# Kernel optimization log

Measured on AMD Instinct MI355X. Metric: run time of the kernel, lower is better.

The kernel has to match this reference:

```python
import jax, jax.numpy as jnp
import numpy as np

B, T, S, V, D, H = 32, 50, 40, 32000, 512, 1024


def setup_inputs() -> dict:
    key = jax.random.key(0)
    ks = jax.random.split(key, 14)
    s_ih = 1.0 / np.sqrt(H)
    return {
        "zh_gruths": jax.random.randint(ks[0], (B, T), 0, V),
        "encoder_hs": jax.random.normal(ks[1], (B, S, H), jnp.float32),
        "encoder_h_n": jax.random.normal(ks[2], (1, B, H), jnp.float32) * 0.1,
        "encoder_c_n": jax.random.normal(ks[3], (1, B, H), jnp.float32) * 0.1,
        "entext_len": jax.random.randint(ks[4], (B,), 1, S + 1),
        "teacher_forcing_ratio": 1,
        "emb": jax.random.normal(ks[5], (V, D), jnp.float32) * 0.02,
        "W_ih": jax.random.normal(ks[6], (4 * H, D), jnp.float32) * s_ih,
        "W_hh": jax.random.normal(ks[7], (4 * H, H), jnp.float32) * s_ih,
        "b_ih": jax.random.normal(ks[8], (4 * H,), jnp.float32) * s_ih,
        "b_hh": jax.random.normal(ks[9], (4 * H,), jnp.float32) * s_ih,
        "W_ht": jax.random.normal(ks[10], (H, 2 * H), jnp.float32) * (1.0 / np.sqrt(2 * H)),
        "b_ht": jnp.zeros((H,), jnp.float32),
        "W_voc": jax.random.normal(ks[11], (V, H), jnp.float32) * s_ih,
        "b_voc": jnp.zeros((V,), jnp.float32),
    }


def reference(zh_gruths, encoder_hs, encoder_h_n, encoder_c_n, entext_len,
              teacher_forcing_ratio, emb, W_ih, W_hh, b_ih, b_hh,
              W_ht, b_ht, W_voc, b_voc):
    # teacher_forcing_ratio == 1 -> always teacher forcing (deterministic branch)
    xs = jnp.swapaxes(emb[zh_gruths], 0, 1)  # [T, B, D]
    hx0, cx0 = encoder_h_n[0], encoder_c_n[0]  # [B, H]

    def step(carry, xt):
        hx, cx = carry
        gates = xt @ W_ih.T + b_ih + hx @ W_hh.T + b_hh  # [B, 4H]
        i, f, g, o = jnp.split(gates, 4, axis=-1)  # torch gate order i,f,g,o
        i, f, o = jax.nn.sigmoid(i), jax.nn.sigmoid(f), jax.nn.sigmoid(o)
        cx = f * cx + i * jnp.tanh(g)
        hx = o * jnp.tanh(cx)
        # dot attention over encoder states
        scores = jnp.einsum('bsh,bh->bs', encoder_hs, hx)
        attn = jax.nn.softmax(scores, axis=-1)
        ctx = jnp.einsum('bs,bsh->bh', attn, encoder_hs)
        hx_atten = jnp.tanh(jnp.concatenate([ctx, hx], axis=-1) @ W_ht.T + b_ht)
        logits_t = hx_atten @ W_voc.T + b_voc  # [B, V]
        return (hx, cx), logits_t

    _, logits = jax.lax.scan(step, (hx0, cx0), xs)  # [T, B, V]
    logits = jnp.swapaxes(logits, 0, 1)  # [B, T, V]
    predicts = jnp.argmax(logits, axis=-1)  # [B, T]
    return logits, predicts
```

## Files before the change

kernel.cpp:

```cpp
#include <hip/hip_runtime.h>
#include <math.h>

typedef short bf16x8 __attribute__((ext_vector_type(8)));
typedef float f32x4 __attribute__((ext_vector_type(4)));
typedef float f32x2 __attribute__((ext_vector_type(2)));
typedef unsigned int uint;
typedef uint u32x4 __attribute__((ext_vector_type(4)));
typedef unsigned long long ull;
typedef unsigned short ushort;

#define Bz 32
#define Tz 50
#define Sz 40
#define Vz 32000
#define Dz 512
#define Hz 1024
#define Mz 1600
#define Mp 1664
#define CAP 1024

__device__ __forceinline__ ushort f2bf(float f) {
    uint u = __builtin_bit_cast(uint, f);
    return (ushort)((u + 0x7FFFu + ((u >> 16) & 1u)) >> 16);
}
__device__ __forceinline__ float bf2f(ushort h) {
    uint u = ((uint)h) << 16;
    return __builtin_bit_cast(float, u);
}
__device__ __forceinline__ void splitf(float f, ushort& hi, ushort& lo) {
    uint u = __builtin_bit_cast(uint, f);
    hi = (ushort)(u >> 16);
    float rem = f - __builtin_bit_cast(float, u & 0xFFFF0000u);
    lo = (ushort)(__builtin_bit_cast(uint, rem) >> 16);
}
__device__ __forceinline__ void splitrn(float f, ushort& hi, ushort& lo) {
    hi = f2bf(f);
    lo = f2bf(f - bf2f(hi));
}
__device__ __forceinline__ float sigf(float x) { return 1.f / (1.f + expf(-x)); }

__device__ __forceinline__ uint ld_sc1(const uint* p) {
    uint v;
    asm volatile("global_load_dword %0, %1, off sc0 sc1\n\ts_waitcnt vmcnt(0)"
                 : "=&v"(v) : "v"(p) : "memory");
    return v;
}
__device__ __forceinline__ void st_sc1(uint* p, uint v) {
    asm volatile("global_store_dword %0, %1, off sc0 sc1" :: "v"(p), "v"(v) : "memory");
}

__global__ __launch_bounds__(256) void k_pre(ushort* hxA_hi, ushort* hxA_lo, float* cx,
                                             ushort* AH_hi, ushort* AH_lo, uint* flags,
                                             const float* h0, const float* c0) {
    int gid = blockIdx.x * 256 + threadIdx.x;
    if (gid < 32768) {
        float v = h0[gid];
        ushort hi, lo;
        splitf(v, hi, lo);
        hxA_hi[gid] = hi;
        hxA_lo[gid] = lo;
    } else if (gid < 65536) {
        cx[gid - 32768] = c0[gid - 32768];
    } else if (gid < 196608) {
        int g = gid - 65536;
        AH_hi[(long)Mz * 2048 + g] = 0;
        AH_lo[(long)Mz * 2048 + g] = 0;
    } else if (gid < 196608 + 2048) {
        st_sc1(&flags[gid - 196608], 0u);
    }
}

__global__ __launch_bounds__(256) void k_wsplit(const float* __restrict__ src,
                                                ushort* __restrict__ hi, ushort* __restrict__ lo,
                                                int n4) {
    int stride = gridDim.x * 256;
    for (int i = blockIdx.x * 256 + threadIdx.x; i < n4; i += stride) {
        float4 f = *(const float4*)(src + (long)i * 4);
        float vv[4] = {f.x, f.y, f.z, f.w};
        ushort h[4], l[4];
#pragma unroll
        for (int e = 0; e < 4; ++e) splitf(vv[e], h[e], l[e]);
        uint2 hp, lp;
        hp.x = (uint)h[0] | ((uint)h[1] << 16);
        hp.y = (uint)h[2] | ((uint)h[3] << 16);
        lp.x = (uint)l[0] | ((uint)l[1] << 16);
        lp.y = (uint)l[2] | ((uint)l[3] << 16);
        *(uint2*)(hi + (long)i * 4) = hp;
        *(uint2*)(lo + (long)i * 4) = lp;
    }
}

__global__ __launch_bounds__(256) void k_wbf16(const float* __restrict__ src,
                                               ushort* __restrict__ dst, int n4) {
    int stride = gridDim.x * 256;
    for (int i = blockIdx.x * 256 + threadIdx.x; i < n4; i += stride) {
        float4 f = *(const float4*)(src + (long)i * 4);
        uint2 hp;
        hp.x = (uint)f2bf(f.x) | ((uint)f2bf(f.y) << 16);
        hp.y = (uint)f2bf(f.z) | ((uint)f2bf(f.w) << 16);
        *(uint2*)(dst + (long)i * 4) = hp;
    }
}

__global__ __launch_bounds__(256, 1) void k_xgemm(const float* __restrict__ emb,
                                                  const int* __restrict__ tok,
                                                  const float* __restrict__ Wih,
                                                  const float* __restrict__ bih,
                                                  const float* __restrict__ bhh,
                                                  float* __restrict__ gx) {
    __shared__ ushort sAh[128][40];
    __shared__ ushort sAl[128][40];
    __shared__ ushort sBh[128][40];
    __shared__ ushort sBl[128][40];
    int bid = blockIdx.x;
    int mt = bid >> 5, nt = bid & 31;
    int tid = threadIdx.x;
    int row = tid >> 1, half = tid & 1;
    int wv = tid >> 6, lane = tid & 63;
    int wr = wv >> 1, wc = wv & 1;
    int m0 = wr * 64, n0 = wc * 64;
    int r16 = lane & 15, kg = lane >> 4, k0 = kg * 8;

    f32x4 acc[4][4];
#pragma unroll
    for (int i = 0; i < 4; i++)
#pragma unroll
        for (int j = 0; j < 4; j++) acc[i][j] = (f32x4){0.f, 0.f, 0.f, 0.f};

    int r = mt * 128 + row;
    int tk = (r < Mz) ? tok[r] : 0;
    const float* arow = emb + (long)tk * Dz;
    const float* brow = Wih + (long)(nt * 128 + row) * Dz;

    for (int kb = 0; kb < Dz; kb += 32) {
        {
            ushort hh[16], ll[16];
#pragma unroll
            for (int q = 0; q < 16; q += 4) {
                float4 w4 = (r < Mz) ? *(const float4*)(arow + kb + half * 16 + q)
                                     : (float4){0.f, 0.f, 0.f, 0.f};
                float vv[4] = {w4.x, w4.y, w4.z, w4.w};
#pragma unroll
                for (int e = 0; e < 4; ++e) splitf(vv[e], hh[q + e], ll[q + e]);
            }
            *(uint4*)&sAh[row][half * 16]     = *(uint4*)&hh[0];
            *(uint4*)&sAh[row][half * 16 + 8] = *(uint4*)&hh[8];
            *(uint4*)&sAl[row][half * 16]     = *(uint4*)&ll[0];
            *(uint4*)&sAl[row][half * 16 + 8] = *(uint4*)&ll[8];
        }
        {
            ushort hh[16], ll[16];
#pragma unroll
            for (int q = 0; q < 16; q += 4) {
                float4 w4 = *(const float4*)(brow + kb + half * 16 + q);
                float vv[4] = {w4.x, w4.y, w4.z, w4.w};
#pragma unroll
                for (int e = 0; e < 4; ++e) splitf(vv[e], hh[q + e], ll[q + e]);
            }
            *(uint4*)&sBh[row][half * 16]     = *(uint4*)&hh[0];
            *(uint4*)&sBh[row][half * 16 + 8] = *(uint4*)&hh[8];
            *(uint4*)&sBl[row][half * 16]     = *(uint4*)&ll[0];
            *(uint4*)&sBl[row][half * 16 + 8] = *(uint4*)&ll[8];
        }
        __syncthreads();
        bf16x8 af[4], alf[4], bhf[4], blf[4];
#pragma unroll
        for (int i = 0; i < 4; ++i) {
            af[i]  = *(const bf16x8*)&sAh[m0 + i * 16 + r16][k0];
            alf[i] = *(const bf16x8*)&sAl[m0 + i * 16 + r16][k0];
            bhf[i] = *(const bf16x8*)&sBh[n0 + i * 16 + r16][k0];
            blf[i] = *(const bf16x8*)&sBl[n0 + i * 16 + r16][k0];
        }
#pragma unroll
        for (int i = 0; i < 4; ++i)
#pragma unroll
            for (int jn = 0; jn < 4; ++jn) {
                acc[i][jn] = __builtin_amdgcn_mfma_f32_16x16x32_bf16(af[i],  bhf[jn], acc[i][jn], 0, 0, 0);
                acc[i][jn] = __builtin_amdgcn_mfma_f32_16x16x32_bf16(af[i],  blf[jn], acc[i][jn], 0, 0, 0);
                acc[i][jn] = __builtin_amdgcn_mfma_f32_16x16x32_bf16(alf[i], bhf[jn], acc[i][jn], 0, 0, 0);
            }
        __syncthreads();
    }
#pragma unroll
    for (int i = 0; i < 4; ++i) {
        int gr0 = mt * 128 + m0 + i * 16 + kg * 4;
#pragma unroll
        for (int reg = 0; reg < 4; ++reg) {
            int gr = gr0 + reg;
            if (gr >= Mz) continue;
#pragma unroll
            for (int jn = 0; jn < 4; ++jn) {
                int gc = nt * 128 + n0 + jn * 16 + r16;
                gx[(long)gr * 4096 + gc] = acc[i][jn][reg] + bih[gc] + bhh[gc];
            }
        }
    }
}

__global__ __launch_bounds__(512, 1) void k_recfused7(
    const float* __restrict__ gx,
    const ushort* __restrict__ Whi, const ushort* __restrict__ Wlo,
    ushort* __restrict__ hxA_hi, ushort* __restrict__ hxA_lo,
    float* __restrict__ hxh, float* __restrict__ cx,
    const float* __restrict__ enc,
    ushort* __restrict__ AH_hi, ushort* __restrict__ AH_lo,
    uint* flags,
    const float* __restrict__ Wvoc, ushort* __restrict__ Wvh,
    int do_wsplit) {
    __shared__ u32x4 stg4[8192];
    __shared__ float hxs[Hz];
    __shared__ float sc[64];
    __shared__ float aw[64];
    int wid = blockIdx.x, tid = threadIdx.x;

    if (wid >= 96) {
        if (do_wsplit) {
            int n4 = Vz * Hz / 4;
            int stride = 160 * 512;
            for (int i = (wid - 96) * 512 + tid; i < n4; i += stride) {
                float4 f = *(const float4*)(Wvoc + (long)i * 4);
                uint2 hp;
                hp.x = (uint)f2bf(f.x) | ((uint)f2bf(f.y) << 16);
                hp.y = (uint)f2bf(f.z) | ((uint)f2bf(f.w) << 16);
                *(uint2*)(Wvh + (long)i * 4) = hp;
            }
        }
        return;
    }

    int lane = tid & 63, kh = tid >> 6;

    for (int t = 0; t <= Tz; ++t) {
        if (wid < 64) {
            if (t < Tz) {
                int w = wid;
                int p = t & 1, q = p ^ 1;
                {
                    bool done = false;
                    while (!done) {
                        uint f = 0xFFFFFFFFu;
                        if (lane < 8) f = ld_sc1(&flags[(kh * 8 + lane) * 16]);
                        done = (bool)__all(f >= (uint)t);
                        if (!done) __builtin_amdgcn_s_sleep(1);
                    }
                }
                int kslot = kh * 16 + (lane & 15);
                int rowb = (lane >> 4) * 8;
                const ushort* planes[2] = { hxA_hi + p * 32768, hxA_lo + p * 32768 };
#pragma unroll
                for (int plane = 0; plane < 2; ++plane) {
                    const ushort* b0 = planes[plane] + (long)rowb * 1024 + kslot * 8;
                    u32x4 d0, d1, d2, d3, d4, d5, d6, d7;
                    asm volatile(
                        "global_load_dwordx4 %0, %8, off sc0 sc1\n\t"
                        "global_load_dwordx4 %1, %9, off sc0 sc1\n\t"
                        "global_load_dwordx4 %2, %10, off sc0 sc1\n\t"
                        "global_load_dwordx4 %3, %11, off sc0 sc1\n\t"
                        "global_load_dwordx4 %4, %12, off sc0 sc1\n\t"
                        "global_load_dwordx4 %5, %13, off sc0 sc1\n\t"
                        "global_load_dwordx4 %6, %14, off sc0 sc1\n\t"
                        "global_load_dwordx4 %7, %15, off sc0 sc1\n\t"
                        "s_waitcnt vmcnt(0)"
                        : "=&v"(d0), "=&v"(d1), "=&v"(d2), "=&v"(d3),
                          "=&v"(d4), "=&v"(d5), "=&v"(d6), "=&v"(d7)
                        : "v"(b0), "v"(b0 + 1024), "v"(b0 + 2048), "v"(b0 + 3072),
                          "v"(b0 + 4096), "v"(b0 + 5120), "v"(b0 + 6144), "v"(b0 + 7168)
                        : "memory");
                    int li = plane * 4096 + kslot * 32;
                    stg4[li + ((rowb + 0 + kslot) & 31)] = d0;
                    stg4[li + ((rowb + 1 + kslot) & 31)] = d1;
                    stg4[li + ((rowb + 2 + kslot) & 31)] = d2;
                    stg4[li + ((rowb + 3 + kslot) & 31)] = d3;
                    stg4[li + ((rowb + 4 + kslot) & 31)] = d4;
                    stg4[li + ((rowb + 5 + kslot) & 31)] = d5;
                    stg4[li + ((rowb + 6 + kslot) & 31)] = d6;
                    stg4[li + ((rowb + 7 + kslot) & 31)] = d7;
                }
                int r16 = lane & 15, kg = lane >> 4;
                int jbase = w * 16 + r16;
                const ushort* whbase = Whi + (long)jbase * 1024;
                const ushort* wlbase = Wlo + (long)jbase * 1024;
                f32x4 acc[2][4];
#pragma unroll
                for (int i = 0; i < 2; ++i)
#pragma unroll
                    for (int v = 0; v < 4; ++v) acc[i][v] = (f32x4){0.f, 0.f, 0.f, 0.f};
#pragma unroll
                for (int it = 0; it < 4; ++it) {
                    int ksl = kh * 16 + it * 4 + kg;
                    int k0 = ksl * 8;
                    bf16x8 a_h0 = *(const bf16x8*)&stg4[       ksl * 32 + ((r16 + ksl) & 31)];
                    bf16x8 a_l0 = *(const bf16x8*)&stg4[4096 + ksl * 32 + ((r16 + ksl) & 31)];
                    bf16x8 a_h1 = *(const bf16x8*)&stg4[       ksl * 32 + ((16 + r16 + ksl) & 31)];
                    bf16x8 a_l1 = *(const bf16x8*)&stg4[4096 + ksl * 32 + ((16 + r16 + ksl) & 31)];
                    bf16x8 bh[4], bl[4];
#pragma unroll
                    for (int v = 0; v < 4; ++v) {
                        bh[v] = *(const bf16x8*)(whbase + ((long)v << 20) + k0);
                        bl[v] = *(const bf16x8*)(wlbase + ((long)v << 20) + k0);
                    }
#pragma unroll
                    for (int v = 0; v < 4; ++v) {
                        acc[0][v] = __builtin_amdgcn_mfma_f32_16x16x32_bf16(a_h0, bh[v], acc[0][v], 0, 0, 0);
                        acc[0][v] = __builtin_amdgcn_mfma_f32_16x16x32_bf16(a_l0, bh[v], acc[0][v], 0, 0, 0);
                        acc[0][v] = __builtin_amdgcn_mfma_f32_16x16x32_bf16(a_h0, bl[v], acc[0][v], 0, 0, 0);
                        acc[1][v] = __builtin_amdgcn_mfma_f32_16x16x32_bf16(a_h1, bh[v], acc[1][v], 0, 0, 0);
                        acc[1][v] = __builtin_amdgcn_mfma_f32_16x16x32_bf16(a_l1, bh[v], acc[1][v], 0, 0, 0);
                        acc[1][v] = __builtin_amdgcn_mfma_f32_16x16x32_bf16(a_h1, bl[v], acc[1][v], 0, 0, 0);
                    }
                }
                __syncthreads();
                float* sgp = (float*)stg4;
#pragma unroll
                for (int i = 0; i < 2; ++i)
#pragma unroll
                    for (int v = 0; v < 4; ++v)
#pragma unroll
                        for (int reg = 0; reg < 4; ++reg)
                            sgp[(((kh * 4 + v) * 32) + i * 16 + kg * 4 + reg) * 16 + r16] = acc[i][v][reg];
                __syncthreads();
                int b = tid >> 4, h16 = tid & 15;
                int hg = w * 16 + h16;
                const float* gxr = gx + ((long)b * Tz + t) * 4096 + hg;
                float g0 = 0.f, g1 = 0.f, g2 = 0.f, g3 = 0.f;
#pragma unroll
                for (int khh = 0; khh < 8; ++khh) {
                    g0 += sgp[((khh * 4 + 0) * 32 + b) * 16 + h16];
                    g1 += sgp[((khh * 4 + 1) * 32 + b) * 16 + h16];
                    g2 += sgp[((khh * 4 + 2) * 32 + b) * 16 + h16];
                    g3 += sgp[((khh * 4 + 3) * 32 + b) * 16 + h16];
                }
                g0 += gxr[0]; g1 += gxr[1024]; g2 += gxr[2048]; g3 += gxr[3072];
                long ci = (long)b * Hz + hg;
                float c = sigf(g1) * cx[ci] + sigf(g0) * tanhf(g2);
                float hv = sigf(g3) * tanhf(c);
                cx[ci] = c;
                float* hp = hxh + ((long)t * Bz + b) * Hz + hg;
                asm volatile("global_store_dword %0, %1, off sc0 sc1" :: "v"(hp), "v"(hv));
                ushort hi, lo;
                splitf(hv, hi, lo);
                ushort* hip = hxA_hi + q * 32768 + ci;
                ushort* lop = hxA_lo + q * 32768 + ci;
                asm volatile("global_store_short %0, %1, off sc0 sc1" :: "v"(hip), "v"((uint)hi));
                asm volatile("global_store_short %0, %1, off sc0 sc1" :: "v"(lop), "v"((uint)lo));
                asm volatile("s_waitcnt vmcnt(0)" ::: "memory");
                __syncthreads();
                if (tid == 0) st_sc1(&flags[wid * 16], (uint)(t + 1));
            }
        } else {
            if (t > 0) {
                int b = wid - 64, tt = t - 1;
                if (tid < 64) {
                    bool done = false;
                    while (!done) {
                        uint f = ld_sc1(&flags[tid * 16]);
                        done = (bool)__all(f >= (uint)t);
                        if (!done) __builtin_amdgcn_s_sleep(2);
                    }
                }
                __syncthreads();
                const float* hsrc = hxh + ((long)tt * Bz + b) * Hz + tid * 2;
                f32x2 h2;
                asm volatile("global_load_dwordx2 %0, %1, off sc0 sc1\n\ts_waitcnt vmcnt(0)"
                             : "=&v"(h2) : "v"(hsrc) : "memory");
                hxs[tid * 2] = h2[0];
                hxs[tid * 2 + 1] = h2[1];
                __syncthreads();
                int wv = tid >> 6;
                float hreg[16];
#pragma unroll
                for (int u = 0; u < 16; ++u) hreg[u] = hxs[lane * 16 + u];
                const float* eb = enc + (long)b * Sz * Hz;
                for (int s = wv; s < Sz; s += 8) {
                    const float* er = eb + (long)s * Hz + lane * 16;
                    float sum = 0.f;
#pragma unroll
                    for (int qq = 0; qq < 4; ++qq) {
                        float4 e4 = *(const float4*)(er + qq * 4);
                        sum += e4.x * hreg[qq*4] + e4.y * hreg[qq*4+1] + e4.z * hreg[qq*4+2] + e4.w * hreg[qq*4+3];
                    }
#pragma unroll
                    for (int off = 32; off >= 1; off >>= 1) sum += __shfl_xor(sum, off);
                    if (lane == 0) sc[s] = sum;
                }
                __syncthreads();
                if (tid < 64) {
                    float vv = (tid < Sz) ? sc[tid] : -3.402823e38f;
                    float mx = vv;
#pragma unroll
                    for (int off = 32; off >= 1; off >>= 1) mx = fmaxf(mx, __shfl_xor(mx, off));
                    float e = (tid < Sz) ? expf(vv - mx) : 0.f;
                    float ssum = e;
#pragma unroll
                    for (int off = 32; off >= 1; off >>= 1) ssum += __shfl_xor(ssum, off);
                    if (tid < Sz) aw[tid] = e / ssum;
                }
                __syncthreads();
                float c0 = 0.f, c1 = 0.f;
#pragma unroll 4
                for (int s = 0; s < Sz; ++s) {
                    float2 e2 = *(const float2*)(eb + (long)s * Hz + tid * 2);
                    float a = aw[s];
                    c0 += a * e2.x; c1 += a * e2.y;
                }
                long rr = (long)b * Tz + tt;
                ushort* dh = AH_hi + rr * 2048;
                ushort* dl = AH_lo + rr * 2048;
                ushort hi, lo;
                splitf(c0, hi, lo); dh[tid * 2]     = hi; dl[tid * 2]     = lo;
                splitf(c1, hi, lo); dh[tid * 2 + 1] = hi; dl[tid * 2 + 1] = lo;
                splitf(hxs[tid * 2],     hi, lo); dh[1024 + tid * 2]     = hi; dl[1024 + tid * 2]     = lo;
                splitf(hxs[tid * 2 + 1], hi, lo); dh[1024 + tid * 2 + 1] = hi; dl[1024 + tid * 2 + 1] = lo;
            }
        }
    }
}

__global__ __launch_bounds__(256, 1) void k_ht(const ushort* __restrict__ Ah,
                                               const ushort* __restrict__ Al,
                                               const ushort* __restrict__ Bh,
                                               const ushort* __restrict__ Bl,
                                               const float* __restrict__ bht,
                                               ushort* __restrict__ Hh, ushort* __restrict__ Hl) {
    __shared__ ushort sAh[128][40];
    __shared__ ushort sAl[128][40];
    __shared__ ushort sBh[128][40];
    __shared__ ushort sBl[128][40];
    int bid = blockIdx.x;
    int mt = bid >> 3, nt = bid & 7;
    int tid = threadIdx.x;
    int row = tid >> 1, half = tid & 1;
    int wv = tid >> 6, lane = tid & 63;
    int wr = wv >> 1, wc = wv & 1;
    int m0 = wr * 64, n0 = wc * 64;
    int r16 = lane & 15, kg = lane >> 4, k0 = kg * 8;

    f32x4 acc[4][4];
#pragma unroll
    for (int i = 0; i < 4; i++)
#pragma unroll
        for (int j = 0; j < 4; j++) acc[i][j] = (f32x4){0.f, 0.f, 0.f, 0.f};

    long arow = (long)(mt * 128 + row) * 2048;
    long brow = (long)(nt * 128 + row) * 2048;

    for (int kb = 0; kb < 2048; kb += 32) {
        const ushort* pa = Ah + arow + kb + half * 16;
        *(uint4*)&sAh[row][half * 16]     = *(const uint4*)pa;
        *(uint4*)&sAh[row][half * 16 + 8] = *(const uint4*)(pa + 8);
        const ushort* pl = Al + arow + kb + half * 16;
        *(uint4*)&sAl[row][half * 16]     = *(const uint4*)pl;
        *(uint4*)&sAl[row][half * 16 + 8] = *(const uint4*)(pl + 8);
        const ushort* pb = Bh + brow + kb + half * 16;
        *(uint4*)&sBh[row][half * 16]     = *(const uint4*)pb;
        *(uint4*)&sBh[row][half * 16 + 8] = *(const uint4*)(pb + 8);
        const ushort* pc = Bl + brow + kb + half * 16;
        *(uint4*)&sBl[row][half * 16]     = *(const uint4*)pc;
        *(uint4*)&sBl[row][half * 16 + 8] = *(const uint4*)(pc + 8);
        __syncthreads();
        bf16x8 af[4], alf[4], bhf[4], blf[4];
#pragma unroll
        for (int i = 0; i < 4; ++i) {
            af[i]  = *(const bf16x8*)&sAh[m0 + i * 16 + r16][k0];
            alf[i] = *(const bf16x8*)&sAl[m0 + i * 16 + r16][k0];
            bhf[i] = *(const bf16x8*)&sBh[n0 + i * 16 + r16][k0];
            blf[i] = *(const bf16x8*)&sBl[n0 + i * 16 + r16][k0];
        }
#pragma unroll
        for (int i = 0; i < 4; ++i)
#pragma unroll
            for (int jn = 0; jn < 4; ++jn) {
                acc[i][jn] = __builtin_amdgcn_mfma_f32_16x16x32_bf16(af[i],  bhf[jn], acc[i][jn], 0, 0, 0);
                acc[i][jn] = __builtin_amdgcn_mfma_f32_16x16x32_bf16(af[i],  blf[jn], acc[i][jn], 0, 0, 0);
                acc[i][jn] = __builtin_amdgcn_mfma_f32_16x16x32_bf16(alf[i], bhf[jn], acc[i][jn], 0, 0, 0);
            }
        __syncthreads();
    }
#pragma unroll
    for (int i = 0; i < 4; ++i) {
        int gr0 = mt * 128 + m0 + i * 16 + kg * 4;
#pragma unroll
        for (int reg = 0; reg < 4; ++reg) {
            int gr = gr0 + reg;
            bool valid = gr < Mz;
#pragma unroll
            for (int jn = 0; jn < 4; ++jn) {
                int gc = nt * 128 + n0 + jn * 16 + r16;
                float vv = tanhf(acc[i][jn][reg] + bht[gc]);
                ushort hi = 0, lo = 0;
                if (valid) splitrn(vv, hi, lo);
                Hh[(long)gr * Hz + gc] = hi;
                Hl[(long)gr * Hz + gc] = lo;
            }
        }
    }
}

__global__ __launch_bounds__(256, 2) void k_voc4(
    const ushort* __restrict__ Ah, const ushort* __restrict__ Wh,
    const float* __restrict__ bvoc,
    float* __restrict__ out, ull* __restrict__ keys) {
    __shared__ ushort sAh[128][40];
    __shared__ ushort sBh[128][40];
    int bid = blockIdx.x;
    int nt = bid % 250, mg = bid / 250;
    int mt_beg = (mg == 0) ? 0 : 7;
    int mt_end = (mg == 0) ? 7 : 13;
    int tid = threadIdx.x;
    int row = tid >> 1, half = tid & 1;
    int wv = tid >> 6, lane = tid & 63;
    int wr = wv >> 1, wc = wv & 1;
    int m0 = wr * 64, n0 = wc * 64;
    int r16 = lane & 15, kg = lane >> 4, k0 = kg * 8;

    long wrow = (long)(nt * 128 + row) * Hz;
    int vcol_base = nt * 128 + n0;

    for (int mt = mt_beg; mt < mt_end; ++mt) {
        f32x4 acc[4][4];
#pragma unroll
        for (int i = 0; i < 4; i++)
#pragma unroll
            for (int j = 0; j < 4; j++) acc[i][j] = (f32x4){0.f, 0.f, 0.f, 0.f};

        long arow = (long)(mt * 128 + row) * Hz;

        for (int kb = 0; kb < Hz; kb += 32) {
            const ushort* pa = Ah + arow + kb + half * 16;
            *(uint4*)&sAh[row][half * 16]     = *(const uint4*)pa;
            *(uint4*)&sAh[row][half * 16 + 8] = *(const uint4*)(pa + 8);
            const ushort* pb = Wh + wrow + kb + half * 16;
            *(uint4*)&sBh[row][half * 16]     = *(const uint4*)pb;
            *(uint4*)&sBh[row][half * 16 + 8] = *(const uint4*)(pb + 8);
            __syncthreads();
            bf16x8 af[4], bhf[4];
#pragma unroll
            for (int i = 0; i < 4; ++i) {
                af[i]  = *(const bf16x8*)&sAh[m0 + i * 16 + r16][k0];
                bhf[i] = *(const bf16x8*)&sBh[n0 + i * 16 + r16][k0];
            }
#pragma unroll
            for (int i = 0; i < 4; ++i)
#pragma unroll
                for (int jn = 0; jn < 4; ++jn)
                    acc[i][jn] = __builtin_amdgcn_mfma_f32_16x16x32_bf16(af[i], bhf[jn], acc[i][jn], 0, 0, 0);
            __syncthreads();
        }
#pragma unroll
        for (int i = 0; i < 4; ++i) {
            int gr0 = mt * 128 + m0 + i * 16 + kg * 4;
#pragma unroll
            for (int reg = 0; reg < 4; ++reg) {
                int gr = gr0 + reg;
                bool valid = gr < Mz;
                float bestv = -3.402823e38f;
                int bestc = 0;
#pragma unroll
                for (int jn = 0; jn < 4; ++jn) {
                    int gc = vcol_base + jn * 16 + r16;
                    float v = acc[i][jn][reg] + bvoc[gc];
                    if (valid) __builtin_nontemporal_store(v, &out[(long)gr * Vz + gc]);
                    if (v > bestv) { bestv = v; bestc = gc; }
                }
#pragma unroll
                for (int off = 1; off < 16; off <<= 1) {
                    float ov = __shfl_xor(bestv, off);
                    int oc = __shfl_xor(bestc, off);
                    if (ov > bestv || (ov == bestv && oc < bestc)) { bestv = ov; bestc = oc; }
                }
                if (valid && r16 == 0) {
                    uint u = __builtin_bit_cast(uint, bestv);
                    u = (u & 0x80000000u) ? ~u : (u | 0x80000000u);
                    keys[(long)gr * 512 + nt * 2 + wc] = (((ull)u) << 32) | (ull)(65535 - bestc);
                }
            }
        }
    }
}

__global__ __launch_bounds__(256) void k_argmax3(const ull* __restrict__ keys,
                                                 float* __restrict__ amax) {
    int r = blockIdx.x, tid = threadIdx.x;
    ull best = 0;
    for (int j = tid; j < 500; j += 256) {
        ull k = keys[(long)r * 512 + j];
        if (k > best) best = k;
    }
    __shared__ ull sk[256];
    sk[tid] = best;
    __syncthreads();
    for (int s = 128; s > 0; s >>= 1) {
        if (tid < s) { if (sk[tid + s] > sk[tid]) sk[tid] = sk[tid + s]; }
        __syncthreads();
    }
    if (tid == 0) {
        uint e = (uint)(sk[0] >> 32);
        uint orig = (e & 0x80000000u) ? (e & 0x7FFFFFFFu) : ~e;
        amax[r] = __builtin_bit_cast(float, orig);
    }
}

__global__ __launch_bounds__(256) void k_rescan(
    const float* __restrict__ out, const float* __restrict__ amax,
    const ushort* __restrict__ Ah, const ushort* __restrict__ Al,
    const float* __restrict__ Wvoc, const float* __restrict__ bvoc,
    float* __restrict__ pred) {
    int r = blockIdx.x, tid = threadIdx.x;
    __shared__ float arow[Hz];
    __shared__ int cand[CAP];
    __shared__ int ccnt;
    __shared__ float cval[4];
    __shared__ float sv[256];
    __shared__ int   si[256];
    if (tid == 0) ccnt = 0;
    float sq = 0.f;
#pragma unroll
    for (int u = 0; u < 4; ++u) {
        int j = tid + 256 * u;
        float a = bf2f(Ah[(long)r * Hz + j]) + bf2f(Al[(long)r * Hz + j]);
        arow[j] = a;
        sq += a * a;
    }
#pragma unroll
    for (int off = 32; off >= 1; off >>= 1) sq += __shfl_xor(sq, off);
    if ((tid & 63) == 0) cval[tid >> 6] = sq;
    __syncthreads();
    float nrm = sqrtf((cval[0] + cval[1]) + (cval[2] + cval[3]));
    float margin = 0.0094f * nrm + 0.01f;
    float thr = amax[r] - margin;
    __syncthreads();
    const float* rowp = out + (long)r * Vz;
    for (int c = tid; c < Vz; c += 256) {
        float v = rowp[c];
        if (v >= thr) {
            int slot = atomicAdd(&ccnt, 1);
            if (slot < CAP) cand[slot] = c;
        }
    }
    __syncthreads();
    int n = ccnt;
    int besti;
    if (n <= CAP) {
        float bestv = -3.402823e38f;
        besti = 0x7FFFFFFF;
        for (int k = 0; k < n; ++k) {
            int c = cand[k];
            const float* wr = Wvoc + (long)c * Hz;
            float s = 0.f;
#pragma unroll
            for (int u = 0; u < 4; ++u) {
                int j = tid + 256 * u;
                s += arow[j] * wr[j];
            }
#pragma unroll
            for (int off = 32; off >= 1; off >>= 1) s += __shfl_xor(s, off);
            if ((tid & 63) == 0) cval[tid >> 6] = s;
            __syncthreads();
            float tot = (cval[0] + cval[1]) + (cval[2] + cval[3]) + bvoc[c];
            if (tot > bestv || (tot == bestv && c < besti)) { bestv = tot; besti = c; }
            __syncthreads();
        }
    } else {
        float bv = -3.402823e38f;
        int bi = 0x7FFFFFFF;
        for (int c = tid; c < Vz; c += 256) {
            const float* wr = Wvoc + (long)c * Hz;
            float s = 0.f;
            for (int j = 0; j < Hz; j += 4) {
                float4 w4 = *(const float4*)(wr + j);
                s += arow[j] * w4.x + arow[j + 1] * w4.y + arow[j + 2] * w4.z + arow[j + 3] * w4.w;
            }
            s += bvoc[c];
            if (s > bv || (s == bv && c < bi)) { bv = s; bi = c; }
        }
        sv[tid] = bv; si[tid] = bi;
        __syncthreads();
        for (int s2 = 128; s2 > 0; s2 >>= 1) {
            if (tid < s2) {
                if (sv[tid + s2] > sv[tid] ||
                    (sv[tid + s2] == sv[tid] && si[tid + s2] < si[tid])) {
                    sv[tid] = sv[tid + s2]; si[tid] = si[tid + s2];
                }
            }
            __syncthreads();
        }
        besti = si[0];
    }
    if (tid == 0) pred[r] = (float)besti;
}

extern "C" void kernel_launch(void* const* d_in, const int* in_sizes, int n_in,
                              void* d_out, int out_size, void* d_ws, size_t ws_size,
                              hipStream_t stream) {
    const int*   tok  = (const int*)d_in[0];
    const float* enc  = (const float*)d_in[1];
    const float* h0   = (const float*)d_in[2];
    const float* c0   = (const float*)d_in[3];
    const float* emb  = (const float*)d_in[6];
    const float* Wih  = (const float*)d_in[7];
    const float* Whh  = (const float*)d_in[8];
    const float* bih  = (const float*)d_in[9];
    const float* bhh  = (const float*)d_in[10];
    const float* Wht  = (const float*)d_in[11];
    const float* bht  = (const float*)d_in[12];
    const float* Wvoc = (const float*)d_in[13];
    const float* bvoc = (const float*)d_in[14];
    float* out = (float*)d_out;

    char* base = (char*)d_ws;
    size_t off = 0;
    float*  gx      = (float*)(base + off);  off += (size_t)Mz * 4096 * 4;
    ushort* hxA_hi  = (ushort*)(base + off); off += 2 * 32768 * 2;
    ushort* hxA_lo  = (ushort*)(base + off); off += 2 * 32768 * 2;
    float*  cx      = (float*)(base + off);  off += 32768 * 4;
    float*  hxh     = (float*)(base + off);  off += (size_t)Tz * Bz * Hz * 4;
    ushort* AH_hi   = (ushort*)(base + off); off += (size_t)Mp * 2048 * 2;
    ushort* AH_lo   = (ushort*)(base + off); off += (size_t)Mp * 2048 * 2;
    ushort* Whh_hi  = (ushort*)(base + off); off += (size_t)4096 * 1024 * 2;
    ushort* Whh_lo  = (ushort*)(base + off); off += (size_t)4096 * 1024 * 2;
    ushort* Wht_hi  = (ushort*)(base + off); off += (size_t)1024 * 2048 * 2;
    ushort* Wht_lo  = (ushort*)(base + off); off += (size_t)1024 * 2048 * 2;

    const size_t wvh_bytes  = (size_t)Vz * Hz * 2;
    const size_t surv_bytes = (size_t)Mp * 1024 * 2 * 2 + (size_t)Mz * 512 * 8 + 8192 + 8192;
    bool fused = ws_size >= off + wvh_bytes + surv_bytes;

    ushort* Wvh; size_t off2;
    if (fused) {
        Wvh = (ushort*)(base + off);
        off2 = off + wvh_bytes;
    } else {
        Wvh = (ushort*)base;
        off2 = wvh_bytes;
    }
    ushort* HXA_hi  = (ushort*)(base + off2); off2 += (size_t)Mp * 1024 * 2;
    ushort* HXA_lo  = (ushort*)(base + off2); off2 += (size_t)Mp * 1024 * 2;
    ull*    keys    = (ull*)(base + off2);    off2 += (size_t)Mz * 512 * 8;
    float*  amax    = (float*)(base + off2);  off2 += 8192;
    uint*   flags   = (uint*)(base + off2);   off2 += 8192;

    k_pre<<<776, 256, 0, stream>>>(hxA_hi, hxA_lo, cx, AH_hi, AH_lo, flags, h0, c0);
    k_wsplit<<<1024, 256, 0, stream>>>(Whh, Whh_hi, Whh_lo, 4096 * 1024 / 4);
    k_wsplit<<<512, 256, 0, stream>>>(Wht, Wht_hi, Wht_lo, 1024 * 2048 / 4);
    k_xgemm<<<13 * 32, 256, 0, stream>>>(emb, tok, Wih, bih, bhh, gx);

    k_recfused7<<<fused ? 256 : 96, 512, 0, stream>>>(
        gx, Whh_hi, Whh_lo, hxA_hi, hxA_lo, hxh, cx, enc, AH_hi, AH_lo, flags,
        Wvoc, Wvh, fused ? 1 : 0);

    k_ht<<<13 * 8, 256, 0, stream>>>(AH_hi, AH_lo, Wht_hi, Wht_lo, bht, HXA_hi, HXA_lo);
    if (!fused) {
        k_wbf16<<<2048, 256, 0, stream>>>(Wvoc, Wvh, Vz * Hz / 4);
    }
    k_voc4<<<500, 256, 0, stream>>>(HXA_hi, Wvh, bvoc, out, keys);
    k_argmax3<<<Mz, 256, 0, stream>>>(keys, amax);
    k_rescan<<<Mz, 256, 0, stream>>>(out, amax, HXA_hi, HXA_lo, Wvoc, bvoc,
                                     out + (long)Mz * Vz);
}
```

Baseline: 1.073 ms.

## Replace flag-based step sync with sentinel-polled per-step hidden buffers; fuse argmax into rescan

The recurrent kernel no longer spins on per-block step flags. Each timestep's packed hi/lo hidden state goes into its own slot, pre-filled with a sentinel, and consumers poll the data itself until no sentinel remains. This removes the flag round trip and the store drain before signalling, and packs hi/lo into one dword. The separate argmax kernel is folded into the rescan kernel, which now scans only 64-column tiles whose tile max passes the threshold instead of the whole row. In exchange, the pre-kernel must write about 13 MB of sentinels, and correctness now depends on no real value ever matching the sentinel bit pattern.

```diff
diff --git a/kernel.cpp b/kernel.cpp
--- a/kernel.cpp
+++ b/kernel.cpp
@@ -18,6 +18,8 @@
 #define Mz 1600
 #define Mp 1664
 #define CAP 1024
+#define NSLOT 51
+#define SENT 0xFFFFFFFFu
 
 __device__ __forceinline__ ushort f2bf(float f) {
     uint u = __builtin_bit_cast(uint, f);
@@ -39,34 +41,35 @@
 }
 __device__ __forceinline__ float sigf(float x) { return 1.f / (1.f + expf(-x)); }
 
-__device__ __forceinline__ uint ld_sc1(const uint* p) {
-    uint v;
-    asm volatile("global_load_dword %0, %1, off sc0 sc1\n\ts_waitcnt vmcnt(0)"
-                 : "=&v"(v) : "v"(p) : "memory");
-    return v;
-}
-__device__ __forceinline__ void st_sc1(uint* p, uint v) {
-    asm volatile("global_store_dword %0, %1, off sc0 sc1" :: "v"(p), "v"(v) : "memory");
-}
-
-__global__ __launch_bounds__(256) void k_pre(ushort* hxA_hi, ushort* hxA_lo, float* cx,
-                                             ushort* AH_hi, ushort* AH_lo, uint* flags,
+__device__ __forceinline__ uint packHi(uint a, uint b) { return (a >> 16) | (b & 0xFFFF0000u); }
+__device__ __forceinline__ uint packLo(uint a, uint b) { return (a & 0xFFFFu) | (b << 16); }
+__device__ __forceinline__ uint chk4(u32x4 d) {
+    return (uint)((d[0] == SENT) | (d[1] == SENT) | (d[2] == SENT) | (d[3] == SENT));
+}
+
+__global__ __launch_bounds__(256) void k_pre(uint* hxP, float* cx,
+                                             ushort* AH_hi, ushort* AH_lo, float* hxh,
                                              const float* h0, const float* c0) {
-    int gid = blockIdx.x * 256 + threadIdx.x;
-    if (gid < 32768) {
-        float v = h0[gid];
-        ushort hi, lo;
-        splitf(v, hi, lo);
-        hxA_hi[gid] = hi;
-        hxA_lo[gid] = lo;
-    } else if (gid < 65536) {
-        cx[gid - 32768] = c0[gid - 32768];
-    } else if (gid < 196608) {
-        int g = gid - 65536;
-        AH_hi[(long)Mz * 2048 + g] = 0;
-        AH_lo[(long)Mz * 2048 + g] = 0;
-    } else if (gid < 196608 + 2048) {
-        st_sc1(&flags[gid - 196608], 0u);
+    const int S0 = 32768, S1 = 65536, S2 = 196608;
+    const int S3 = S2 + 50 * 32768, S4 = S3 + 50 * 32768;
+    int stride = gridDim.x * 256;
+    for (int gid = blockIdx.x * 256 + threadIdx.x; gid < S4; gid += stride) {
+        if (gid < S0) {
+            float v = h0[gid];
+            ushort hi, lo;
+            splitf(v, hi, lo);
+            hxP[gid] = ((uint)hi << 16) | lo;
+        } else if (gid < S1) {
+            cx[gid - S0] = c0[gid - S0];
+        } else if (gid < S2) {
+            int g = gid - S1;
+            AH_hi[(long)Mz * 2048 + g] = 0;
+            AH_lo[(long)Mz * 2048 + g] = 0;
+        } else if (gid < S3) {
+            hxP[32768 + (gid - S2)] = SENT;
+        } else {
+            ((uint*)hxh)[gid - S3] = SENT;
+        }
     }
 }
 
@@ -197,14 +200,13 @@
     }
 }
 
-__global__ __launch_bounds__(512, 1) void k_recfused7(
+__global__ __launch_bounds__(512, 1) void k_recfused9(
     const float* __restrict__ gx,
     const ushort* __restrict__ Whi, const ushort* __restrict__ Wlo,
-    ushort* __restrict__ hxA_hi, ushort* __restrict__ hxA_lo,
+    uint* __restrict__ hxP,
     float* __restrict__ hxh, float* __restrict__ cx,
     const float* __restrict__ enc,
     ushort* __restrict__ AH_hi, ushort* __restrict__ AH_lo,
-    uint* flags,
     const float* __restrict__ Wvoc, ushort* __restrict__ Wvh,
     int do_wsplit) {
     __shared__ u32x4 stg4[8192];
@@ -234,47 +236,50 @@
         if (wid < 64) {
             if (t < Tz) {
                 int w = wid;
-                int p = t & 1, q = p ^ 1;
-                {
-                    bool done = false;
-                    while (!done) {
-                        uint f = 0xFFFFFFFFu;
-                        if (lane < 8) f = ld_sc1(&flags[(kh * 8 + lane) * 16]);
-                        done = (bool)__all(f >= (uint)t);
-                        if (!done) __builtin_amdgcn_s_sleep(1);
-                    }
-                }
+                long rdoff = (long)t * 32768;
+                long wroff = (long)(t + 1) * 32768;
                 int kslot = kh * 16 + (lane & 15);
                 int rowb = (lane >> 4) * 8;
-                const ushort* planes[2] = { hxA_hi + p * 32768, hxA_lo + p * 32768 };
-#pragma unroll
-                for (int plane = 0; plane < 2; ++plane) {
-                    const ushort* b0 = planes[plane] + (long)rowb * 1024 + kslot * 8;
-                    u32x4 d0, d1, d2, d3, d4, d5, d6, d7;
-                    asm volatile(
-                        "global_load_dwordx4 %0, %8, off sc0 sc1\n\t"
-                        "global_load_dwordx4 %1, %9, off sc0 sc1\n\t"
-                        "global_load_dwordx4 %2, %10, off sc0 sc1\n\t"
-                        "global_load_dwordx4 %3, %11, off sc0 sc1\n\t"
-                        "global_load_dwordx4 %4, %12, off sc0 sc1\n\t"
-                        "global_load_dwordx4 %5, %13, off sc0 sc1\n\t"
-                        "global_load_dwordx4 %6, %14, off sc0 sc1\n\t"
-                        "global_load_dwordx4 %7, %15, off sc0 sc1\n\t"
-                        "s_waitcnt vmcnt(0)"
-                        : "=&v"(d0), "=&v"(d1), "=&v"(d2), "=&v"(d3),
-                          "=&v"(d4), "=&v"(d5), "=&v"(d6), "=&v"(d7)
-                        : "v"(b0), "v"(b0 + 1024), "v"(b0 + 2048), "v"(b0 + 3072),
-                          "v"(b0 + 4096), "v"(b0 + 5120), "v"(b0 + 6144), "v"(b0 + 7168)
-                        : "memory");
-                    int li = plane * 4096 + kslot * 32;
-                    stg4[li + ((rowb + 0 + kslot) & 31)] = d0;
-                    stg4[li + ((rowb + 1 + kslot) & 31)] = d1;
-                    stg4[li + ((rowb + 2 + kslot) & 31)] = d2;
-                    stg4[li + ((rowb + 3 + kslot) & 31)] = d3;
-                    stg4[li + ((rowb + 4 + kslot) & 31)] = d4;
-                    stg4[li + ((rowb + 5 + kslot) & 31)] = d5;
-                    stg4[li + ((rowb + 6 + kslot) & 31)] = d6;
-                    stg4[li + ((rowb + 7 + kslot) & 31)] = d7;
+                const uint* bp = hxP + rdoff + (long)rowb * 1024 + kslot * 8;
+#pragma unroll
+                for (int grp = 0; grp < 2; ++grp) {
+                    const uint* g0 = bp + (long)grp * 4096;
+                    u32x4 a0, b0, a1, b1, a2, b2, a3, b3;
+                    while (1) {
+                        asm volatile(
+                            "global_load_dwordx4 %0, %8, off sc0 sc1\n\t"
+                            "global_load_dwordx4 %1, %9, off sc0 sc1\n\t"
+                            "global_load_dwordx4 %2, %10, off sc0 sc1\n\t"
+                            "global_load_dwordx4 %3, %11, off sc0 sc1\n\t"
+                            "global_load_dwordx4 %4, %12, off sc0 sc1\n\t"
+                            "global_load_dwordx4 %5, %13, off sc0 sc1\n\t"
+                            "global_load_dwordx4 %6, %14, off sc0 sc1\n\t"
+                            "global_load_dwordx4 %7, %15, off sc0 sc1\n\t"
+                            "s_waitcnt vmcnt(0)"
+                            : "=&v"(a0), "=&v"(b0), "=&v"(a1), "=&v"(b1),
+                              "=&v"(a2), "=&v"(b2), "=&v"(a3), "=&v"(b3)
+                            : "v"(g0), "v"(g0 + 4), "v"(g0 + 1024), "v"(g0 + 1028),
+                              "v"(g0 + 2048), "v"(g0 + 2052), "v"(g0 + 3072), "v"(g0 + 3076)
+                            : "memory");
+                        uint bad = chk4(a0) | chk4(b0) | chk4(a1) | chk4(b1)
+                                 | chk4(a2) | chk4(b2) | chk4(a3) | chk4(b3);
+                        if (__all(bad == 0)) break;
+                        __builtin_amdgcn_s_sleep(1);
+                    }
+                    int li = kslot * 32;
+#define STROW(rl, dA, dB)                                                            \
+                    {                                                                \
+                        int rr = rowb + grp * 4 + (rl);                              \
+                        int idx = li + ((rr + kslot) & 31);                          \
+                        u32x4 h4, l4;                                                \
+                        h4[0] = packHi(dA[0], dA[1]); h4[1] = packHi(dA[2], dA[3]);  \
+                        h4[2] = packHi(dB[0], dB[1]); h4[3] = packHi(dB[2], dB[3]);  \
+                        l4[0] = packLo(dA[0], dA[1]); l4[1] = packLo(dA[2], dA[3]);  \
+                        l4[2] = packLo(dB[0], dB[1]); l4[3] = packLo(dB[2], dB[3]);  \
+                        stg4[idx] = h4; stg4[4096 + idx] = l4;                       \
+                    }
+                    STROW(0, a0, b0) STROW(1, a1, b1) STROW(2, a2, b2) STROW(3, a3, b3)
+#undef STROW
                 }
                 int r16 = lane & 15, kg = lane >> 4;
                 int jbase = w * 16 + r16;
@@ -322,47 +327,41 @@
                 int b = tid >> 4, h16 = tid & 15;
                 int hg = w * 16 + h16;
                 const float* gxr = gx + ((long)b * Tz + t) * 4096 + hg;
-                float g0 = 0.f, g1 = 0.f, g2 = 0.f, g3 = 0.f;
+                float g0s = 0.f, g1s = 0.f, g2s = 0.f, g3s = 0.f;
 #pragma unroll
                 for (int khh = 0; khh < 8; ++khh) {
-                    g0 += sgp[((khh * 4 + 0) * 32 + b) * 16 + h16];
-                    g1 += sgp[((khh * 4 + 1) * 32 + b) * 16 + h16];
-                    g2 += sgp[((khh * 4 + 2) * 32 + b) * 16 + h16];
-                    g3 += sgp[((khh * 4 + 3) * 32 + b) * 16 + h16];
-                }
-                g0 += gxr[0]; g1 += gxr[1024]; g2 += gxr[2048]; g3 += gxr[3072];
+                    g0s += sgp[((khh * 4 + 0) * 32 + b) * 16 + h16];
+                    g1s += sgp[((khh * 4 + 1) * 32 + b) * 16 + h16];
+                    g2s += sgp[((khh * 4 + 2) * 32 + b) * 16 + h16];
+                    g3s += sgp[((khh * 4 + 3) * 32 + b) * 16 + h16];
+                }
+                g0s += gxr[0]; g1s += gxr[1024]; g2s += gxr[2048]; g3s += gxr[3072];
                 long ci = (long)b * Hz + hg;
-                float c = sigf(g1) * cx[ci] + sigf(g0) * tanhf(g2);
-                float hv = sigf(g3) * tanhf(c);
+                float c = sigf(g1s) * cx[ci] + sigf(g0s) * tanhf(g2s);
+                float hv = sigf(g3s) * tanhf(c);
                 cx[ci] = c;
                 float* hp = hxh + ((long)t * Bz + b) * Hz + hg;
                 asm volatile("global_store_dword %0, %1, off sc0 sc1" :: "v"(hp), "v"(hv));
                 ushort hi, lo;
                 splitf(hv, hi, lo);
-                ushort* hip = hxA_hi + q * 32768 + ci;
-                ushort* lop = hxA_lo + q * 32768 + ci;
-                asm volatile("global_store_short %0, %1, off sc0 sc1" :: "v"(hip), "v"((uint)hi));
-                asm volatile("global_store_short %0, %1, off sc0 sc1" :: "v"(lop), "v"((uint)lo));
-                asm volatile("s_waitcnt vmcnt(0)" ::: "memory");
+                uint pk = ((uint)hi << 16) | lo;
+                uint* pp = hxP + wroff + ci;
+                asm volatile("global_store_dword %0, %1, off sc0 sc1" :: "v"(pp), "v"(pk));
                 __syncthreads();
-                if (tid == 0) st_sc1(&flags[wid * 16], (uint)(t + 1));
             }
         } else {
             if (t > 0) {
                 int b = wid - 64, tt = t - 1;
-                if (tid < 64) {
-                    bool done = false;
-                    while (!done) {
-                        uint f = ld_sc1(&flags[tid * 16]);
-                        done = (bool)__all(f >= (uint)t);
-                        if (!done) __builtin_amdgcn_s_sleep(2);
-                    }
-                }
-                __syncthreads();
                 const float* hsrc = hxh + ((long)tt * Bz + b) * Hz + tid * 2;
                 f32x2 h2;
-                asm volatile("global_load_dwordx2 %0, %1, off sc0 sc1\n\ts_waitcnt vmcnt(0)"
-                             : "=&v"(h2) : "v"(hsrc) : "memory");
+                while (1) {
+                    asm volatile("global_load_dwordx2 %0, %1, off sc0 sc1\n\ts_waitcnt vmcnt(0)"
+                                 : "=&v"(h2) : "v"(hsrc) : "memory");
+                    uint u0 = __builtin_bit_cast(uint, h2[0]);
+                    uint u1 = __builtin_bit_cast(uint, h2[1]);
+                    if (u0 != SENT && u1 != SENT) break;
+                    __builtin_amdgcn_s_sleep(2);
+                }
                 hxs[tid * 2] = h2[0];
                 hxs[tid * 2 + 1] = h2[1];
                 __syncthreads();
@@ -411,6 +410,7 @@
                 splitf(c1, hi, lo); dh[tid * 2 + 1] = hi; dl[tid * 2 + 1] = lo;
                 splitf(hxs[tid * 2],     hi, lo); dh[1024 + tid * 2]     = hi; dl[1024 + tid * 2]     = lo;
                 splitf(hxs[tid * 2 + 1], hi, lo); dh[1024 + tid * 2 + 1] = hi; dl[1024 + tid * 2 + 1] = lo;
+                __syncthreads();
             }
         }
     }
@@ -578,30 +578,8 @@
     }
 }
 
-__global__ __launch_bounds__(256) void k_argmax3(const ull* __restrict__ keys,
-                                                 float* __restrict__ amax) {
-    int r = blockIdx.x, tid = threadIdx.x;
-    ull best = 0;
-    for (int j = tid; j < 500; j += 256) {
-        ull k = keys[(long)r * 512 + j];
-        if (k > best) best = k;
-    }
-    __shared__ ull sk[256];
-    sk[tid] = best;
-    __syncthreads();
-    for (int s = 128; s > 0; s >>= 1) {
-        if (tid < s) { if (sk[tid + s] > sk[tid]) sk[tid] = sk[tid + s]; }
-        __syncthreads();
-    }
-    if (tid == 0) {
-        uint e = (uint)(sk[0] >> 32);
-        uint orig = (e & 0x80000000u) ? (e & 0x7FFFFFFFu) : ~e;
-        amax[r] = __builtin_bit_cast(float, orig);
-    }
-}
-
-__global__ __launch_bounds__(256) void k_rescan(
-    const float* __restrict__ out, const float* __restrict__ amax,
+__global__ __launch_bounds__(256) void k_rescan2(
+    const float* __restrict__ out, const ull* __restrict__ keys,
     const ushort* __restrict__ Ah, const ushort* __restrict__ Al,
     const float* __restrict__ Wvoc, const float* __restrict__ bvoc,
     float* __restrict__ pred) {
@@ -610,6 +588,7 @@
     __shared__ int cand[CAP];
     __shared__ int ccnt;
     __shared__ float cval[4];
+    __shared__ ull sk[256];
     __shared__ float sv[256];
     __shared__ int   si[256];
     if (tid == 0) ccnt = 0;
@@ -624,17 +603,38 @@
 #pragma unroll
     for (int off = 32; off >= 1; off >>= 1) sq += __shfl_xor(sq, off);
     if ((tid & 63) == 0) cval[tid >> 6] = sq;
+    ull best = 0;
+    for (int j = tid; j < 500; j += 256) {
+        ull k = keys[(long)r * 512 + j];
+        if (k > best) best = k;
+    }
+    sk[tid] = best;
     __syncthreads();
+    for (int s = 128; s > 0; s >>= 1) {
+        if (tid < s) { if (sk[tid + s] > sk[tid]) sk[tid] = sk[tid + s]; }
+        __syncthreads();
+    }
+    uint e0 = (uint)(sk[0] >> 32);
+    uint ob0 = (e0 & 0x80000000u) ? (e0 & 0x7FFFFFFFu) : ~e0;
+    float amaxv = __builtin_bit_cast(float, ob0);
     float nrm = sqrtf((cval[0] + cval[1]) + (cval[2] + cval[3]));
     float margin = 0.0094f * nrm + 0.01f;
-    float thr = amax[r] - margin;
+    float thr = amaxv - margin;
     __syncthreads();
-    const float* rowp = out + (long)r * Vz;
-    for (int c = tid; c < Vz; c += 256) {
-        float v = rowp[c];
-        if (v >= thr) {
-            int slot = atomicAdd(&ccnt, 1);
-            if (slot < CAP) cand[slot] = c;
+    for (int j = tid; j < 500; j += 256) {
+        ull k = keys[(long)r * 512 + j];
+        uint e = (uint)(k >> 32);
+        uint ob = (e & 0x80000000u) ? (e & 0x7FFFFFFFu) : ~e;
+        float tv = __builtin_bit_cast(float, ob);
+        if (tv >= thr) {
+            int cb = (j >> 1) * 128 + (j & 1) * 64;
+            for (int c2 = 0; c2 < 64; ++c2) {
+                float v = out[(long)r * Vz + cb + c2];
+                if (v >= thr) {
+                    int slot = atomicAdd(&ccnt, 1);
+                    if (slot < CAP) cand[slot] = cb + c2;
+                }
+            }
         }
     }
     __syncthreads();
@@ -710,8 +710,7 @@
     char* base = (char*)d_ws;
     size_t off = 0;
     float*  gx      = (float*)(base + off);  off += (size_t)Mz * 4096 * 4;
-    ushort* hxA_hi  = (ushort*)(base + off); off += 2 * 32768 * 2;
-    ushort* hxA_lo  = (ushort*)(base + off); off += 2 * 32768 * 2;
+    uint*   hxP     = (uint*)(base + off);   off += (size_t)NSLOT * 32768 * 4;
     float*  cx      = (float*)(base + off);  off += 32768 * 4;
     float*  hxh     = (float*)(base + off);  off += (size_t)Tz * Bz * Hz * 4;
     ushort* AH_hi   = (ushort*)(base + off); off += (size_t)Mp * 2048 * 2;
@@ -722,7 +721,7 @@
     ushort* Wht_lo  = (ushort*)(base + off); off += (size_t)1024 * 2048 * 2;
 
     const size_t wvh_bytes  = (size_t)Vz * Hz * 2;
-    const size_t surv_bytes = (size_t)Mp * 1024 * 2 * 2 + (size_t)Mz * 512 * 8 + 8192 + 8192;
+    const size_t surv_bytes = (size_t)Mp * 1024 * 2 * 2 + (size_t)Mz * 512 * 8 + 8192;
     bool fused = ws_size >= off + wvh_bytes + surv_bytes;
 
     ushort* Wvh; size_t off2;
@@ -736,24 +735,20 @@
     ushort* HXA_hi  = (ushort*)(base + off2); off2 += (size_t)Mp * 1024 * 2;
     ushort* HXA_lo  = (ushort*)(base + off2); off2 += (size_t)Mp * 1024 * 2;
     ull*    keys    = (ull*)(base + off2);    off2 += (size_t)Mz * 512 * 8;
-    float*  amax    = (float*)(base + off2);  off2 += 8192;
-    uint*   flags   = (uint*)(base + off2);   off2 += 8192;
-
-    k_pre<<<776, 256, 0, stream>>>(hxA_hi, hxA_lo, cx, AH_hi, AH_lo, flags, h0, c0);
+
+    k_pre<<<4096, 256, 0, stream>>>(hxP, cx, AH_hi, AH_lo, hxh, h0, c0);
     k_wsplit<<<1024, 256, 0, stream>>>(Whh, Whh_hi, Whh_lo, 4096 * 1024 / 4);
     k_wsplit<<<512, 256, 0, stream>>>(Wht, Wht_hi, Wht_lo, 1024 * 2048 / 4);
     k_xgemm<<<13 * 32, 256, 0, stream>>>(emb, tok, Wih, bih, bhh, gx);
 
-    k_recfused7<<<fused ? 256 : 96, 512, 0, stream>>>(
-        gx, Whh_hi, Whh_lo, hxA_hi, hxA_lo, hxh, cx, enc, AH_hi, AH_lo, flags,
-        Wvoc, Wvh, fused ? 1 : 0);
+    k_recfused9<<<fused ? 256 : 96, 512, 0, stream>>>(
+        gx, Whh_hi, Whh_lo, hxP, hxh, cx, enc, AH_hi, AH_lo, Wvoc, Wvh, fused ? 1 : 0);
 
     k_ht<<<13 * 8, 256, 0, stream>>>(AH_hi, AH_lo, Wht_hi, Wht_lo, bht, HXA_hi, HXA_lo);
     if (!fused) {
         k_wbf16<<<2048, 256, 0, stream>>>(Wvoc, Wvh, Vz * Hz / 4);
     }
     k_voc4<<<500, 256, 0, stream>>>(HXA_hi, Wvh, bvoc, out, keys);
-    k_argmax3<<<Mz, 256, 0, stream>>>(keys, amax);
-    k_rescan<<<Mz, 256, 0, stream>>>(out, amax, HXA_hi, HXA_lo, Wvoc, bvoc,
-                                     out + (long)Mz * Vz);
-}
+    k_rescan2<<<Mz, 256, 0, stream>>>(out, keys, HXA_hi, HXA_lo, Wvoc, bvoc,
+                                      out + (long)Mz * Vz);
+}
```

Result: faster. 982.8 us (-8.4%).
